# Kernel optimization log

Hardware: AMD Instinct MI355X
Metric: run time of the kernel (lower is better)

Reference implementation:

```python
import jax, jax.numpy as jnp
import numpy as np

NCE_T = 0.07  # opt.nce_T
EPS = 1e-8    # torch CosineSimilarity eps

def setup_inputs() -> dict:
    key = jax.random.key(0)
    k1, k2, k3 = jax.random.split(key, 3)
    num_patches, C = 4096, 256
    features = jax.random.normal(k1, (2, num_patches, C), dtype=jnp.float32)
    labels_seg = jax.random.randint(k2, (1, 1, 128, 128, 128), 0, 5, dtype=jnp.int32)
    labels_coords = jax.random.randint(k3, (num_patches, 3), 0, 64, dtype=jnp.int32)
    return {"features": features, "labels_seg": labels_seg,
            "labels_coords": labels_coords, "cr_w": 64, "cr_h": 64, "cr_d": 64}

def _sup_nce_loss(features, lab):
    # features: (ntps, N, C); lab: (N,) int class per patch
    ntps, N, C = features.shape
    M = ntps * N
    f = features.reshape(M, C)
    nrm = jnp.linalg.norm(f, axis=-1)  # (M,)
    # cosine similarity = (f @ f^T) / max(|x||y|, eps), then / temperature
    sim = (f @ f.T) / jnp.maximum(nrm[:, None] * nrm[None, :], EPS)
    logits = sim / NCE_T
    logits = logits - jax.lax.stop_gradient(jnp.max(logits, axis=1, keepdims=True))
    pos = (lab[:, None] == lab[None, :]).astype(f.dtype)        # (N,N)
    pos = jnp.tile(pos, (ntps, ntps))                            # (M,M)
    diag_off = 1.0 - jnp.eye(M, dtype=f.dtype)                   # logits_mask
    pos = pos * diag_off
    denom = jnp.log((jnp.exp(logits) * diag_off).sum(1, keepdims=True))
    log_prob = logits - denom
    mean_log_prob_pos = (pos * log_prob).sum(1) / pos.sum(1)
    return -(mean_log_prob_pos.reshape(ntps, N)).mean()

def reference(features, labels_seg, labels_coords, cr_w, cr_h, cr_d):
    # nearest-neighbor downsample of labels to coords_range (torch 'nearest': floor(i*in/out))
    H, W, D = labels_seg.shape[2], labels_seg.shape[3], labels_seg.shape[4]
    iw = (jnp.arange(cr_w) * H) // cr_w
    ih = (jnp.arange(cr_h) * W) // cr_h
    idd = (jnp.arange(cr_d) * D) // cr_d
    seg = labels_seg[0, 0][iw][:, ih][:, :, idd]  # (cr_w, cr_h, cr_d)
    lab = seg[labels_coords[:, 0], labels_coords[:, 1], labels_coords[:, 2]]  # (N,)
    return _sup_nce_loss(features, lab)
```

## Files before the change

kernel.cpp:

```cpp
#include <hip/hip_runtime.h>
#include <hip/hip_bf16.h>

typedef __attribute__((ext_vector_type(4))) float floatx4;

#define C_DIM 256
#define INV_T 14.285714285714286f
#define K2_SCALE 20.60992915f

__device__ __forceinline__ unsigned int pack4fp8(float a, float b, float c, float d) {
    int w = __builtin_amdgcn_cvt_pk_fp8_f32(a, b, 0, false);
    w = __builtin_amdgcn_cvt_pk_fp8_f32(c, d, w, true);
    return (unsigned int)w;
}

template <int CTRL>
__device__ __forceinline__ float dppadd(float x) {
    int y = __builtin_amdgcn_update_dpp(0, __builtin_bit_cast(int, x),
                                        CTRL, 0xf, 0xf, true);
    return x + __builtin_bit_cast(float, y);
}
__device__ __forceinline__ float row16_sum(float x) {
    x = dppadd<0xB1>(x);
    x = dppadd<0x4E>(x);
    x = dppadd<0x124>(x);
    x = dppadd<0x128>(x);
    return x;
}

__global__ __launch_bounds__(256) void
norm_kernel(const float* __restrict__ f,
            unsigned char* __restrict__ g2,
            const int* __restrict__ seg,
            const int* __restrict__ coords,
            const int* __restrict__ crw,
            const int* __restrict__ crh,
            const int* __restrict__ crd,
            int* __restrict__ lab,
            float* __restrict__ Spart,
            int* __restrict__ histpart,
            float* __restrict__ acc_done,
            int N, int H, int W, int D) {
    __shared__ float nrm[16][264];
    __shared__ float Sloc[5][256];
    __shared__ int lbl[16];
    __shared__ int histloc[8];

    const int tid = threadIdx.x;
    const int bid = blockIdx.x;
    const int lane = tid & 63;
    const int wave = tid >> 6;
    const int rbase = bid * 32;

    if (bid == 0 && tid == 0) {
        acc_done[0] = 0.0f;
        ((int*)acc_done)[1] = 0;
    }
    if (tid < 8) histloc[tid] = 0;
#pragma unroll
    for (int c = 0; c < 5; ++c) Sloc[c][tid] = 0.0f;
    __syncthreads();

    for (int g = 0; g < 2; ++g) {
        const int grow0 = rbase + g * 16;
        if (tid < 16) {
            const int row = grow0 + tid;
            const int p = row & (N - 1);
            int c0 = coords[3 * p + 0];
            int c1 = coords[3 * p + 1];
            int c2 = coords[3 * p + 2];
            int i0 = (c0 * H) / crw[0];
            int i1 = (c1 * W) / crh[0];
            int i2 = (c2 * D) / crd[0];
            const int c = seg[(i0 * W + i1) * D + i2];
            lbl[tid] = c;
            if (row < N) {
                lab[row] = c;
                atomicAdd(&histloc[c], 1);
            }
        }
        const int rl = wave * 4;
#pragma unroll
        for (int q = 0; q < 4; ++q) {
            const int row = grow0 + rl + q;
            const float4 v = ((const float4*)(f + (size_t)row * C_DIM))[lane];
            float ss = v.x * v.x + v.y * v.y + v.z * v.z + v.w * v.w;
#pragma unroll
            for (int off = 32; off; off >>= 1) ss += __shfl_xor(ss, off, 64);
            const float inv = 1.0f / sqrtf(ss);
            *(float4*)&nrm[rl + q][lane * 4] =
                float4{v.x * inv, v.y * inv, v.z * inv, v.w * inv};
        }
        __syncthreads();

        const int k0 = (tid >> 5) * 32 + ((tid >> 3) & 3) * 8;
        const float* ra = &nrm[(2 * tid) & 15][k0];
        const float* rb = &nrm[(2 * tid + 1) & 15][k0];
        uint4 o;
        o.x = pack4fp8(ra[0], ra[1], ra[2], ra[3]);
        o.y = pack4fp8(ra[4], ra[5], ra[6], ra[7]);
        o.z = pack4fp8(rb[0], rb[1], rb[2], rb[3]);
        o.w = pack4fp8(rb[4], rb[5], rb[6], rb[7]);
        *(uint4*)(g2 + (size_t)(bid * 2 + g) * 4096 + (size_t)tid * 16) = o;

#pragma unroll
        for (int rr = 0; rr < 16; ++rr)
            Sloc[lbl[rr]][tid] += nrm[rr][tid];
        __syncthreads();
    }

#pragma unroll
    for (int c = 0; c < 5; ++c)
        Spart[(size_t)bid * 1280 + c * 256 + tid] = Sloc[c][tid];
    if (tid < 8) histpart[bid * 8 + tid] = histloc[tid];
}

__global__ __launch_bounds__(256, 2) void
gram_kernel(const unsigned char* __restrict__ G2,
            float* __restrict__ part,
            int M, int nt) {
    __shared__ unsigned char Abuf[32768];
    __shared__ unsigned char Bbuf[32768];
    __shared__ float red[2][2][128];

    const int tid = threadIdx.x;
    const int bid = blockIdx.x;
    const int lane = tid & 63;
    const int wave = tid >> 6;
    const int waveM = wave >> 1;
    const int waveN = wave & 1;
    const int cc = lane & 15;
    const int cq = lane >> 4;

    const int start = bid * 4 + (bid < 32 ? bid : 32);
    const int len = 4 + (bid < 32 ? 1 : 0);
    int tmPrev = -1;

    for (int s = 0; s < len; ++s) {
        const int idx = start + s;
        float fnt = (float)nt;
        float disc = (2.0f * fnt + 1.0f) * (2.0f * fnt + 1.0f) - 8.0f * (float)idx;
        int tm = (int)((2.0f * fnt + 1.0f - sqrtf(disc)) * 0.5f);
        if (tm < 0) tm = 0;
        if (tm > nt - 1) tm = nt - 1;
        while (tm > 0 && idx < tm * nt - tm * (tm - 1) / 2) --tm;
        while (idx >= (tm + 1) * nt - (tm + 1) * tm / 2) ++tm;
        const int tn = tm + (idx - (tm * nt - tm * (tm - 1) / 2));

        const int rowA0 = tm * 128;
        const int rowB0 = tn * 128;
        const bool diagTile = (tm == tn);

        if (tm != tmPrev) {
            const unsigned char* gA = G2 + (size_t)tm * 32768;
#pragma unroll
            for (int i = 0; i < 8; ++i) {
                const int u = i * 256 + tid;
                __builtin_amdgcn_global_load_lds(
                    (const __attribute__((address_space(1))) void*)(gA + (size_t)u * 16),
                    (__attribute__((address_space(3))) void*)(&Abuf[(u & ~63) * 16]),
                    16, 0, 0);
            }
            tmPrev = tm;
        }
        if (!diagTile) {
            const unsigned char* gB = G2 + (size_t)tn * 32768;
#pragma unroll
            for (int i = 0; i < 8; ++i) {
                const int u = i * 256 + tid;
                __builtin_amdgcn_global_load_lds(
                    (const __attribute__((address_space(1))) void*)(gB + (size_t)u * 16),
                    (__attribute__((address_space(3))) void*)(&Bbuf[(u & ~63) * 16]),
                    16, 0, 0);
            }
        }
        __syncthreads();

        const unsigned char* A = Abuf;
        const unsigned char* B = diagTile ? Abuf : Bbuf;

        floatx4 acc[4][4];
#pragma unroll
        for (int mi = 0; mi < 4; ++mi)
#pragma unroll
            for (int ni = 0; ni < 4; ++ni)
                acc[mi][ni] = floatx4{-1.0f, -1.0f, -1.0f, -1.0f};

#pragma unroll
        for (int ks = 0; ks < 8; ++ks) {
            long af[4], bf[4];
#pragma unroll
            for (int mi = 0; mi < 4; ++mi)
                af[mi] = *(const long*)&A[(size_t)((waveM * 4 + mi) * 8 + ks) * 512 + lane * 8];
#pragma unroll
            for (int ni = 0; ni < 4; ++ni)
                bf[ni] = *(const long*)&B[(size_t)((waveN * 4 + ni) * 8 + ks) * 512 + lane * 8];
#pragma unroll
            for (int mi = 0; mi < 4; ++mi)
#pragma unroll
                for (int ni = 0; ni < 4; ++ni)
                    acc[mi][ni] = __builtin_amdgcn_mfma_f32_16x16x32_fp8_fp8(
                        af[mi], bf[ni], acc[mi][ni], 0, 0, 0);
        }

        if (!diagTile) {
            float bse[4] = {};
#pragma unroll
            for (int mi = 0; mi < 4; ++mi) {
#pragma unroll
                for (int r = 0; r < 4; ++r) {
                    const int lrow = waveM * 64 + mi * 16 + cq * 4 + r;
                    float se = 0.0f;
#pragma unroll
                    for (int ni = 0; ni < 4; ++ni) {
                        const float e = exp2f(acc[mi][ni][r] * K2_SCALE);
                        se += e;
                        bse[ni] += e;
                    }
                    se = row16_sum(se);
                    if (cc == 0) red[0][waveN][lrow] = se;
                }
            }
#pragma unroll
            for (int ni = 0; ni < 4; ++ni) {
                float se = bse[ni];
                se += __shfl_xor(se, 16, 64);
                se += __shfl_xor(se, 32, 64);
                if (cq == 0) red[1][waveM][waveN * 64 + ni * 16 + cc] = se;
            }
        } else {
#pragma unroll
            for (int mi = 0; mi < 4; ++mi) {
#pragma unroll
                for (int r = 0; r < 4; ++r) {
                    const int lrow = waveM * 64 + mi * 16 + cq * 4 + r;
                    const int grow = rowA0 + lrow;
                    float se = 0.0f;
#pragma unroll
                    for (int ni = 0; ni < 4; ++ni) {
                        const int gcol = rowB0 + waveN * 64 + ni * 16 + cc;
                        const float e = exp2f(acc[mi][ni][r] * K2_SCALE);
                        se += (gcol != grow) ? e : 0.0f;
                    }
                    se = row16_sum(se);
                    if (cc == 0) red[0][waveN][lrow] = se;
                }
            }
        }
        __syncthreads();

        if (tid < 128)
            part[(size_t)tn * M + rowA0 + tid] = red[0][0][tid] + red[0][1][tid];
        if (!diagTile && tid >= 128)
            part[(size_t)tm * M + rowB0 + (tid - 128)] =
                red[1][0][tid - 128] + red[1][1][tid - 128];
        __syncthreads();
    }
}

__global__ __launch_bounds__(256) void
finalize_kernel(const float* __restrict__ part,
                const float* __restrict__ Spart,
                const int* __restrict__ histpart,
                float* __restrict__ acc_done,
                float* __restrict__ out,
                int M, int N, int nslots, int fblk) {
    __shared__ float sred[256];
    __shared__ int hred[256];

    const int tid = threadIdx.x;
    const int bid = blockIdx.x;
    const int ntps = M / N;
    const int nblk = fblk + 5;
    float blocksum = 0.0f;

    if (bid < fblk) {
        const int r0 = bid * 256;
        float se = 0.0f;
        for (int s = 0; s < nslots; ++s) se += part[(size_t)s * M + r0 + tid];
        sred[tid] = -logf(se);
        __syncthreads();
        for (int k = 128; k; k >>= 1) {
            if (tid < k) sred[tid] += sred[tid + k];
            __syncthreads();
        }
        blocksum = sred[0];
    } else {
        const int c = bid - fblk;
        float a0 = 0.0f, a1 = 0.0f, a2 = 0.0f, a3 = 0.0f;
        float a4 = 0.0f, a5 = 0.0f, a6 = 0.0f, a7 = 0.0f;
        const float* Sp = Spart + c * 256 + tid;
        for (int b = 0; b < 256; b += 8) {
            a0 += Sp[(size_t)(b + 0) * 1280];
            a1 += Sp[(size_t)(b + 1) * 1280];
            a2 += Sp[(size_t)(b + 2) * 1280];
            a3 += Sp[(size_t)(b + 3) * 1280];
            a4 += Sp[(size_t)(b + 4) * 1280];
            a5 += Sp[(size_t)(b + 5) * 1280];
            a6 += Sp[(size_t)(b + 6) * 1280];
            a7 += Sp[(size_t)(b + 7) * 1280];
        }
        const float v = ((a0 + a1) + (a2 + a3)) + ((a4 + a5) + (a6 + a7));
        sred[tid] = v * v;
        hred[tid] = histpart[tid * 8 + c];
        __syncthreads();
        for (int k = 128; k; k >>= 1) {
            if (tid < k) {
                sred[tid] += sred[tid + k];
                hred[tid] += hred[tid + k];
            }
            __syncthreads();
        }
        if (tid == 0) {
            const float S2 = sred[0];
            const float Mc = (float)(ntps * hred[0]);
            const float cnt = Mc - 1.0f;
            float contrib = (cnt > 0.0f) ? INV_T * (S2 - Mc) / cnt : 0.0f;
            if (c == 0) contrib -= INV_T * (float)M;
            blocksum = contrib;
        }
    }

    if (tid == 0) {
        atomicAdd(&acc_done[0], blocksum);
        __threadfence();
        int old = atomicAdd((int*)&acc_done[1], 1);
        if (old == nblk - 1) {
            float total = atomicAdd(&acc_done[0], 0.0f);
            out[0] = -total / (float)M;
        }
    }
}

extern "C" void kernel_launch(void* const* d_in, const int* in_sizes, int n_in,
                              void* d_out, int out_size, void* d_ws, size_t ws_size,
                              hipStream_t stream) {
    const float* features = (const float*)d_in[0];
    const int* labels_seg = (const int*)d_in[1];
    const int* labels_coords = (const int*)d_in[2];
    const int* crw = (const int*)d_in[3];
    const int* crh = (const int*)d_in[4];
    const int* crd = (const int*)d_in[5];
    float* out = (float*)d_out;

    const int N = in_sizes[2] / 3;
    const int M = in_sizes[0] / C_DIM;
    const int H = 128, W = 128, D = 128;
    const int nt = M / 128;

    char* ws = (char*)d_ws;
    unsigned char* g2 = (unsigned char*)ws;
    char* p1 = ws + (size_t)M * C_DIM;
    int* lab = (int*)p1;
    char* p2 = p1 + (size_t)N * 4;
    float* part = (float*)p2;
    char* p3 = p2 + (size_t)nt * M * 4;
    float* Spart = (float*)p3;
    char* p4 = p3 + (size_t)256 * 1280 * 4;
    int* histpart = (int*)p4;
    float* acc_done = (float*)(p4 + 256 * 8 * 4);

    norm_kernel<<<M / 32, 256, 0, stream>>>(features, g2, labels_seg,
                                            labels_coords, crw, crh, crd, lab,
                                            Spart, histpart, acc_done,
                                            N, H, W, D);

    gram_kernel<<<512, 256, 0, stream>>>(g2, part, M, nt);

    const int fblk = M / 256;
    finalize_kernel<<<fblk + 5, 256, 0, stream>>>(part, Spart, histpart,
                                                  acc_done, out, M, N, nt, fblk);
}
```

Measured before the change: 122.6 us.

## Prefetch next gram tile into LDS during exp epilogue

The gram kernel now decodes the next triangular tile index and issues the async global-to-LDS loads for its A/B panels right after the MFMA loop finishes, so the loads overlap the exp/row-sum epilogue and the partial-sum stores. The first tile is loaded before the loop, and the barrier placement moves so operand buffers are only overwritten after every wave has finished reading them. This trades some reordering risk (the red buffer and its barriers must still protect the epilogue) for hiding global load latency between tiles.

Result: no change. 120.4 us (-1.7%).

```diff
diff --git a/kernel.cpp b/kernel.cpp
--- a/kernel.cpp
+++ b/kernel.cpp
@@ -25,6 +25,18 @@
     x = dppadd<0x124>(x);
     x = dppadd<0x128>(x);
     return x;
+}
+
+__device__ __forceinline__ void decode_tile(int idx, int nt, int& tm, int& tn) {
+    float fnt = (float)nt;
+    float disc = (2.0f * fnt + 1.0f) * (2.0f * fnt + 1.0f) - 8.0f * (float)idx;
+    int t = (int)((2.0f * fnt + 1.0f - sqrtf(disc)) * 0.5f);
+    if (t < 0) t = 0;
+    if (t > nt - 1) t = nt - 1;
+    while (t > 0 && idx < t * nt - t * (t - 1) / 2) --t;
+    while (idx >= (t + 1) * nt - (t + 1) * t / 2) ++t;
+    tm = t;
+    tn = t + (idx - (t * nt - t * (t - 1) / 2));
 }
 
 __global__ __launch_bounds__(256) void
@@ -133,37 +145,22 @@
 
     const int start = bid * 4 + (bid < 32 ? bid : 32);
     const int len = 4 + (bid < 32 ? 1 : 0);
-    int tmPrev = -1;
-
-    for (int s = 0; s < len; ++s) {
-        const int idx = start + s;
-        float fnt = (float)nt;
-        float disc = (2.0f * fnt + 1.0f) * (2.0f * fnt + 1.0f) - 8.0f * (float)idx;
-        int tm = (int)((2.0f * fnt + 1.0f - sqrtf(disc)) * 0.5f);
-        if (tm < 0) tm = 0;
-        if (tm > nt - 1) tm = nt - 1;
-        while (tm > 0 && idx < tm * nt - tm * (tm - 1) / 2) --tm;
-        while (idx >= (tm + 1) * nt - (tm + 1) * tm / 2) ++tm;
-        const int tn = tm + (idx - (tm * nt - tm * (tm - 1) / 2));
-
-        const int rowA0 = tm * 128;
-        const int rowB0 = tn * 128;
-        const bool diagTile = (tm == tn);
-
-        if (tm != tmPrev) {
-            const unsigned char* gA = G2 + (size_t)tm * 32768;
-#pragma unroll
-            for (int i = 0; i < 8; ++i) {
-                const int u = i * 256 + tid;
-                __builtin_amdgcn_global_load_lds(
-                    (const __attribute__((address_space(1))) void*)(gA + (size_t)u * 16),
-                    (__attribute__((address_space(3))) void*)(&Abuf[(u & ~63) * 16]),
-                    16, 0, 0);
-            }
-            tmPrev = tm;
-        }
-        if (!diagTile) {
-            const unsigned char* gB = G2 + (size_t)tn * 32768;
+
+    int tmCur, tnCur;
+    decode_tile(start, nt, tmCur, tnCur);
+
+    {
+        const unsigned char* gA = G2 + (size_t)tmCur * 32768;
+#pragma unroll
+        for (int i = 0; i < 8; ++i) {
+            const int u = i * 256 + tid;
+            __builtin_amdgcn_global_load_lds(
+                (const __attribute__((address_space(1))) void*)(gA + (size_t)u * 16),
+                (__attribute__((address_space(3))) void*)(&Abuf[(u & ~63) * 16]),
+                16, 0, 0);
+        }
+        if (tnCur != tmCur) {
+            const unsigned char* gB = G2 + (size_t)tnCur * 32768;
 #pragma unroll
             for (int i = 0; i < 8; ++i) {
                 const int u = i * 256 + tid;
@@ -173,10 +170,17 @@
                     16, 0, 0);
             }
         }
-        __syncthreads();
-
+    }
+
+    for (int s = 0; s < len; ++s) {
+        const int tm = tmCur, tn = tnCur;
+        const int rowA0 = tm * 128;
+        const int rowB0 = tn * 128;
+        const bool diagTile = (tm == tn);
         const unsigned char* A = Abuf;
         const unsigned char* B = diagTile ? Abuf : Bbuf;
+
+        __syncthreads();
 
         floatx4 acc[4][4];
 #pragma unroll
@@ -200,6 +204,37 @@
                 for (int ni = 0; ni < 4; ++ni)
                     acc[mi][ni] = __builtin_amdgcn_mfma_f32_16x16x32_fp8_fp8(
                         af[mi], bf[ni], acc[mi][ni], 0, 0, 0);
+        }
+
+        __syncthreads();
+
+        if (s + 1 < len) {
+            int tmN, tnN;
+            decode_tile(start + s + 1, nt, tmN, tnN);
+            if (tmN != tm) {
+                const unsigned char* gA = G2 + (size_t)tmN * 32768;
+#pragma unroll
+                for (int i = 0; i < 8; ++i) {
+                    const int u = i * 256 + tid;
+                    __builtin_amdgcn_global_load_lds(
+                        (const __attribute__((address_space(1))) void*)(gA + (size_t)u * 16),
+                        (__attribute__((address_space(3))) void*)(&Abuf[(u & ~63) * 16]),
+                        16, 0, 0);
+                }
+            }
+            if (tnN != tmN) {
+                const unsigned char* gB = G2 + (size_t)tnN * 32768;
+#pragma unroll
+                for (int i = 0; i < 8; ++i) {
+                    const int u = i * 256 + tid;
+                    __builtin_amdgcn_global_load_lds(
+                        (const __attribute__((address_space(1))) void*)(gB + (size_t)u * 16),
+                        (__attribute__((address_space(3))) void*)(&Bbuf[(u & ~63) * 16]),
+                        16, 0, 0);
+                }
+            }
+            tmCur = tmN;
+            tnCur = tnN;
         }
 
         if (!diagTile) {
@@ -253,7 +288,6 @@
         if (!diagTile && tid >= 128)
             part[(size_t)tm * M + rowB0 + (tid - 128)] =
                 red[1][0][tid - 128] + red[1][1][tid - 128];
-        __syncthreads();
     }
 }
 
```
